# Kernel tuning notes

Hardware: AMD Instinct MI355X
Metric: run time of the kernel (lower is better)

## Reference

```python
import jax, jax.numpy as jnp
import numpy as np

K = 1  # number of items to sample exactly
B, N = 512, 8192


def log1mexp(x):
    # log(1 - exp(x)) for x <= 0, numerically stable (Maechler 2012)
    return jnp.where(x > -jnp.log(2.0), jnp.log(-jnp.expm1(x)), jnp.log1p(-jnp.exp(x)))


def logaddexp_c(x1, x2):
    # custom logaddexp matching the torch module (handles -inf == -inf ties)
    delta = jnp.where(x1 == x2, 0.0, x1 - x2)
    return jnp.maximum(x1, x2) + jax.nn.softplus(-jnp.abs(delta))


def dp_table(logp, logq, kk):
    # a[b, i, c] = log Pr(exactly c-1 successes among first i items); shape [B, n+1, kk+2]
    bsz = logp.shape[0]
    state0 = jnp.full((bsz, kk + 2), -jnp.inf, logp.dtype).at[:, 1].set(0.0)
    ninf_col = jnp.full((bsz, 1), -jnp.inf, logp.dtype)

    def step(state, xs):
        lp, lq = xs  # each [B]
        grown = logaddexp_c(state[:, :-1] + lp[:, None], state[:, 1:] + lq[:, None])
        new = jnp.concatenate([ninf_col, grown], axis=1)
        return new, new

    _, rows = jax.lax.scan(step, state0, (logp.T, logq.T))  # rows: [n, B, kk+2]
    return jnp.concatenate([state0[None], rows], axis=0).transpose(1, 0, 2)


def sample_scan(a, logp, noise):
    # reverse DP sampling pass; a: [B, n+1, C], logp/noise: [B, n]
    bsz, np1, C = a.shape
    n = np1 - 1
    kcol = C - 1  # == K + 1 in table-column coordinates
    ap = a[:, :-1, :][:, ::-1].transpose(1, 0, 2)  # [n, B, C], row i-1 for i=n..1
    ac = a[:, 1:, :][:, ::-1].transpose(1, 0, 2)   # [n, B, C], row i   for i=n..1
    lp_rev = logp[:, ::-1].T                        # [n, B]
    u_rev = noise[:, ::-1].T                        # [n, B]

    def step(j, xs):
        ap_r, ac_r, lp_t, u_t = xs
        p = jnp.take_along_axis(ap_r, (j - 1)[:, None], axis=1)[:, 0]
        z = jnp.take_along_axis(ac_r, j[:, None], axis=1)[:, 0]
        p = jnp.minimum(p + lp_t - z, 0.0)  # conditional log-prob, clamp fp round-off
        q = log1mexp(p)
        X = (u_t < jax.nn.sigmoid(p - q)).astype(logp.dtype)  # Bernoulli(logits=p-q)
        j = jnp.where(X > 0, j - 1, j)
        return j, X

    j0 = jnp.full((bsz,), kcol, jnp.int32)
    _, Xs = jax.lax.scan(step, j0, (ap, ac, lp_rev, u_rev))  # Xs: [n, B]
    return Xs[::-1].T  # [B, n]


def setup_inputs() -> dict:
    key = jax.random.key(0)
    k1, k2 = jax.random.split(key)
    logits = jax.random.normal(k1, (B, N), dtype=jnp.float32)
    noise = jax.random.uniform(k2, (B, N), dtype=jnp.float32)
    return {"logits": logits, "noise": noise}


def reference(logits, noise):
    logp = jnp.minimum(jax.nn.log_sigmoid(logits), -1e-7)  # clamped log_sigmoid
    logq = log1mexp(logp)
    a = dp_table(logp, logq, K)       # [B, N+1, K+2]
    return sample_scan(a, logp, noise)  # [B, N] in {0,1}
```

## Files before the change

### kernel.cpp

```cpp
#include <hip/hip_runtime.h>
#include <math.h>

#define NB 512
#define NI 8192
#define NLOG2 0.69314718055994530942f

__device__ __forceinline__ float log1mexp_f(float x) {
    return (x > -NLOG2) ? logf(-expm1f(x)) : log1pf(-expf(x));
}

__global__ __launch_bounds__(256) void prep_kernel(const float* __restrict__ logits,
                                                   float* __restrict__ Alp,
                                                   float* __restrict__ Blq) {
    int idx = blockIdx.x * blockDim.x + threadIdx.x;
    float4 x4 = ((const float4*)logits)[idx];
    float4 lp4, lq4;
    const float* xs = &x4.x;
    float* lps = &lp4.x;
    float* lqs = &lq4.x;
#pragma unroll
    for (int j = 0; j < 4; ++j) {
        float x = xs[j];
        float lp = -(fmaxf(-x, 0.0f) + log1pf(expf(-fabsf(x))));
        lp = fminf(lp, -1e-7f);
        lps[j] = lp;
        lqs[j] = log1mexp_f(lp);
    }
    ((float4*)Alp)[idx] = lp4;
    ((float4*)Blq)[idx] = lq4;
}

#define CH 32
__device__ __forceinline__ void scan_step(float lp, float lq, float& S0, float& S1,
                                          float& x1o, float& s1o) {
    const float L2E = 1.44269504088896340736f;
    const float LN2 = 0.69314718055994530942f;
    float x1 = S0 + lp;
    float x2 = S1 + lq;
    float d  = x1 - x2;
    float m  = fmaxf(x1, x2);
    float z  = fabsf(d) * -L2E;
    float e  = __builtin_amdgcn_exp2f(z);
    float a  = 1.0f + e;
    float l  = __builtin_amdgcn_logf(a);
    S1 = fmaf(l, LN2, m);
    S0 = S0 + lq;
    x1o = x1;
    s1o = S1;
}

__global__ __launch_bounds__(64, 1) void scan_kernel(float* __restrict__ A,
                                                     float* __restrict__ B) {
    int row = blockIdx.x * blockDim.x + threadIdx.x;
    float* Ar = A + (size_t)row * NI;
    float* Br = B + (size_t)row * NI;

    float S0 = 0.0f;
    float S1 = -INFINITY;

    float lpA[CH], lqA[CH], lpB[CH], lqB[CH];
    float x1A[CH], s1A[CH], x1B[CH], s1B[CH];

#pragma unroll
    for (int j = 0; j < CH / 4; ++j) {
        *(float4*)&lpA[4 * j] = *(const float4*)&Ar[4 * j];
        *(float4*)&lqA[4 * j] = *(const float4*)&Br[4 * j];
    }

    const int NCHUNK = NI / CH;
    for (int c = 0; c < NCHUNK; c += 2) {
        const int base0 = c * CH, base1 = (c + 1) * CH, base2 = (c + 2) * CH;

#pragma unroll
        for (int j = 0; j < CH / 4; ++j) {
            *(float4*)&lpB[4 * j] = *(const float4*)&Ar[base1 + 4 * j];
            *(float4*)&lqB[4 * j] = *(const float4*)&Br[base1 + 4 * j];
        }

#pragma unroll
        for (int j = 0; j < CH; ++j)
            scan_step(lpA[j], lqA[j], S0, S1, x1A[j], s1A[j]);
#pragma unroll
        for (int j = 0; j < CH / 4; ++j) {
            *(float4*)&Ar[base0 + 4 * j] = *(float4*)&x1A[4 * j];
            *(float4*)&Br[base0 + 4 * j] = *(float4*)&s1A[4 * j];
        }

        if (c + 2 < NCHUNK) {
#pragma unroll
            for (int j = 0; j < CH / 4; ++j) {
                *(float4*)&lpA[4 * j] = *(const float4*)&Ar[base2 + 4 * j];
                *(float4*)&lqA[4 * j] = *(const float4*)&Br[base2 + 4 * j];
            }
        }

#pragma unroll
        for (int j = 0; j < CH; ++j)
            scan_step(lpB[j], lqB[j], S0, S1, x1B[j], s1B[j]);
#pragma unroll
        for (int j = 0; j < CH / 4; ++j) {
            *(float4*)&Ar[base1 + 4 * j] = *(float4*)&x1B[4 * j];
            *(float4*)&Br[base1 + 4 * j] = *(float4*)&s1B[4 * j];
        }
    }
}

__global__ __launch_bounds__(256) void decide_kernel(const float* __restrict__ A,
                                                     const float* __restrict__ S,
                                                     const float* __restrict__ noise,
                                                     float* __restrict__ out) {
    int row = blockIdx.x;
    const float4* x1r = (const float4*)(A + (size_t)row * NI);
    const float4* s1r = (const float4*)(S + (size_t)row * NI);
    const float4* ur = (const float4*)(noise + (size_t)row * NI);
    float4* outr = (float4*)(out + (size_t)row * NI);
    int tid = threadIdx.x;

    int best = -1;
#pragma unroll
    for (int k = 0; k < NI / 4 / 256; ++k) {
        int g = tid + k * 256;
        float4 x1 = x1r[g];
        float4 s1 = s1r[g];
        float4 u = ur[g];
#pragma unroll
        for (int j = 0; j < 4; ++j) {
            float p = fminf((&x1.x)[j] - (&s1.x)[j], 0.0f);
            float q = log1mexp_f(p);
            float z = p - q;
            float prob = 1.0f / (1.0f + expf(-z));
            if ((&u.x)[j] < prob) {
                int i = 4 * g + j;
                best = (i > best) ? i : best;
            }
        }
    }

#pragma unroll
    for (int off = 32; off > 0; off >>= 1) {
        int o = __shfl_down(best, off);
        best = (o > best) ? o : best;
    }
    __shared__ int lds[4];
    __shared__ int sel_s;
    int wid = tid >> 6;
    if ((tid & 63) == 0) lds[wid] = best;
    __syncthreads();
    if (tid == 0) {
        int s01 = (lds[0] > lds[1]) ? lds[0] : lds[1];
        int s23 = (lds[2] > lds[3]) ? lds[2] : lds[3];
        sel_s = (s01 > s23) ? s01 : s23;
    }
    __syncthreads();
    int sel = sel_s;

#pragma unroll
    for (int k = 0; k < NI / 4 / 256; ++k) {
        int g = tid + k * 256;
        int i0 = 4 * g;
        float4 v;
        v.x = (i0 == sel) ? 1.0f : 0.0f;
        v.y = (i0 + 1 == sel) ? 1.0f : 0.0f;
        v.z = (i0 + 2 == sel) ? 1.0f : 0.0f;
        v.w = (i0 + 3 == sel) ? 1.0f : 0.0f;
        outr[g] = v;
    }
}

extern "C" void kernel_launch(void* const* d_in, const int* in_sizes, int n_in,
                              void* d_out, int out_size, void* d_ws, size_t ws_size,
                              hipStream_t stream) {
    (void)in_sizes; (void)n_in; (void)out_size; (void)ws_size;
    const float* logits = (const float*)d_in[0];
    const float* noise = (const float*)d_in[1];
    float* out = (float*)d_out;
    float* A = (float*)d_ws;

    int total4 = NB * NI / 4;
    prep_kernel<<<total4 / 256, 256, 0, stream>>>(logits, A, out);
    scan_kernel<<<8, 64, 0, stream>>>(A, out);
    decide_kernel<<<NB, 256, 0, stream>>>(A, out, noise, out);
}
```

Measured before the change: 485.2 us.

## Transpose DP scratch to item-major layout for coalesced scan-kernel access

The prep kernel now transposes log-probabilities through shared memory into an item-major [NI/4][NB] float4 layout. The sequential scan kernel's 64 lanes then read and write adjacent rows, so its memory accesses coalesce instead of being strided by a full row. The decide kernel reads the transposed layout, which is strided per row. The output write is moved into a separate kernel because the decide kernel's reads and the final writes share the out buffer, and the selected index is passed through a global array.

```diff
diff --git a/kernel.cpp b/kernel.cpp
--- a/kernel.cpp
+++ b/kernel.cpp
@@ -3,34 +3,61 @@
 
 #define NB 512
 #define NI 8192
+#define NG (NI / 4)
 #define NLOG2 0.69314718055994530942f
 
 __device__ __forceinline__ float log1mexp_f(float x) {
     return (x > -NLOG2) ? logf(-expm1f(x)) : log1pf(-expf(x));
 }
 
+__device__ int g_sel[NB];
+
+#define TB 64
+#define TK 16
 __global__ __launch_bounds__(256) void prep_kernel(const float* __restrict__ logits,
                                                    float* __restrict__ Alp,
                                                    float* __restrict__ Blq) {
-    int idx = blockIdx.x * blockDim.x + threadIdx.x;
-    float4 x4 = ((const float4*)logits)[idx];
-    float4 lp4, lq4;
-    const float* xs = &x4.x;
-    float* lps = &lp4.x;
-    float* lqs = &lq4.x;
-#pragma unroll
-    for (int j = 0; j < 4; ++j) {
-        float x = xs[j];
-        float lp = -(fmaxf(-x, 0.0f) + log1pf(expf(-fabsf(x))));
-        lp = fminf(lp, -1e-7f);
-        lps[j] = lp;
-        lqs[j] = log1mexp_f(lp);
-    }
-    ((float4*)Alp)[idx] = lp4;
-    ((float4*)Blq)[idx] = lq4;
-}
-
-#define CH 32
+    __shared__ float4 lp_t[TB][TK + 1];
+    __shared__ float4 lq_t[TB][TK + 1];
+    int bx = blockIdx.x;
+    int tb = (bx & 7) * TB;
+    int tkb = (bx >> 3) * TK;
+    int t = threadIdx.x;
+
+    int kl = t & 15;
+    int rl0 = t >> 4;
+#pragma unroll
+    for (int r = 0; r < 4; ++r) {
+        int row_local = r * 16 + rl0;
+        float4 x4 = *(const float4*)&logits[(size_t)(tb + row_local) * NI + (size_t)(tkb + kl) * 4];
+        float4 lp4, lq4;
+        const float* xs = &x4.x;
+        float* lps = &lp4.x;
+        float* lqs = &lq4.x;
+#pragma unroll
+        for (int j = 0; j < 4; ++j) {
+            float x = xs[j];
+            float lp = -(fmaxf(-x, 0.0f) + log1pf(expf(-fabsf(x))));
+            lp = fminf(lp, -1e-7f);
+            lps[j] = lp;
+            lqs[j] = log1mexp_f(lp);
+        }
+        lp_t[row_local][kl] = lp4;
+        lq_t[row_local][kl] = lq4;
+    }
+    __syncthreads();
+
+    int bl = t & 63;
+    int kw0 = t >> 6;
+#pragma unroll
+    for (int w = 0; w < 4; ++w) {
+        int k_local = w * 4 + kw0;
+        size_t dst = (size_t)(tkb + k_local) * NB + (size_t)(tb + bl);
+        ((float4*)Alp)[dst] = lp_t[bl][k_local];
+        ((float4*)Blq)[dst] = lq_t[bl][k_local];
+    }
+}
+
 __device__ __forceinline__ void scan_step(float lp, float lq, float& S0, float& S1,
                                           float& x1o, float& s1o) {
     const float L2E = 1.44269504088896340736f;
@@ -49,79 +76,86 @@
     s1o = S1;
 }
 
+__device__ __forceinline__ void scan_step4(float4 lp, float4 lq, float& S0, float& S1,
+                                           float4& x1v, float4& s1v) {
+    scan_step(lp.x, lq.x, S0, S1, x1v.x, s1v.x);
+    scan_step(lp.y, lq.y, S0, S1, x1v.y, s1v.y);
+    scan_step(lp.z, lq.z, S0, S1, x1v.z, s1v.z);
+    scan_step(lp.w, lq.w, S0, S1, x1v.w, s1v.w);
+}
+
+#define SD 8
 __global__ __launch_bounds__(64, 1) void scan_kernel(float* __restrict__ A,
                                                      float* __restrict__ B) {
-    int row = blockIdx.x * blockDim.x + threadIdx.x;
-    float* Ar = A + (size_t)row * NI;
-    float* Br = B + (size_t)row * NI;
+    int row = blockIdx.x * 64 + threadIdx.x;
+    float4* Ap = (float4*)A;
+    float4* Bp = (float4*)B;
 
     float S0 = 0.0f;
     float S1 = -INFINITY;
 
-    float lpA[CH], lqA[CH], lpB[CH], lqB[CH];
-    float x1A[CH], s1A[CH], x1B[CH], s1B[CH];
-
-#pragma unroll
-    for (int j = 0; j < CH / 4; ++j) {
-        *(float4*)&lpA[4 * j] = *(const float4*)&Ar[4 * j];
-        *(float4*)&lqA[4 * j] = *(const float4*)&Br[4 * j];
-    }
-
-    const int NCHUNK = NI / CH;
+    float4 lpA[SD], lqA[SD], lpB[SD], lqB[SD];
+
+#pragma unroll
+    for (int j = 0; j < SD; ++j) {
+        lpA[j] = Ap[(size_t)j * NB + row];
+        lqA[j] = Bp[(size_t)j * NB + row];
+    }
+
+    const int NCHUNK = NG / SD;
     for (int c = 0; c < NCHUNK; c += 2) {
-        const int base0 = c * CH, base1 = (c + 1) * CH, base2 = (c + 2) * CH;
-
-#pragma unroll
-        for (int j = 0; j < CH / 4; ++j) {
-            *(float4*)&lpB[4 * j] = *(const float4*)&Ar[base1 + 4 * j];
-            *(float4*)&lqB[4 * j] = *(const float4*)&Br[base1 + 4 * j];
-        }
-
-#pragma unroll
-        for (int j = 0; j < CH; ++j)
-            scan_step(lpA[j], lqA[j], S0, S1, x1A[j], s1A[j]);
-#pragma unroll
-        for (int j = 0; j < CH / 4; ++j) {
-            *(float4*)&Ar[base0 + 4 * j] = *(float4*)&x1A[4 * j];
-            *(float4*)&Br[base0 + 4 * j] = *(float4*)&s1A[4 * j];
+        size_t g1 = (size_t)(c + 1) * SD;
+        size_t g2 = (size_t)(c + 2) * SD;
+
+#pragma unroll
+        for (int j = 0; j < SD; ++j) {
+            lpB[j] = Ap[(g1 + j) * NB + row];
+            lqB[j] = Bp[(g1 + j) * NB + row];
+        }
+
+#pragma unroll
+        for (int j = 0; j < SD; ++j) {
+            float4 x1v, s1v;
+            scan_step4(lpA[j], lqA[j], S0, S1, x1v, s1v);
+            size_t g = (size_t)c * SD + j;
+            Ap[g * NB + row] = x1v;
+            Bp[g * NB + row] = s1v;
         }
 
         if (c + 2 < NCHUNK) {
 #pragma unroll
-            for (int j = 0; j < CH / 4; ++j) {
-                *(float4*)&lpA[4 * j] = *(const float4*)&Ar[base2 + 4 * j];
-                *(float4*)&lqA[4 * j] = *(const float4*)&Br[base2 + 4 * j];
+            for (int j = 0; j < SD; ++j) {
+                lpA[j] = Ap[(g2 + j) * NB + row];
+                lqA[j] = Bp[(g2 + j) * NB + row];
             }
         }
 
 #pragma unroll
-        for (int j = 0; j < CH; ++j)
-            scan_step(lpB[j], lqB[j], S0, S1, x1B[j], s1B[j]);
-#pragma unroll
-        for (int j = 0; j < CH / 4; ++j) {
-            *(float4*)&Ar[base1 + 4 * j] = *(float4*)&x1B[4 * j];
-            *(float4*)&Br[base1 + 4 * j] = *(float4*)&s1B[4 * j];
+        for (int j = 0; j < SD; ++j) {
+            float4 x1v, s1v;
+            scan_step4(lpB[j], lqB[j], S0, S1, x1v, s1v);
+            size_t g = g1 + j;
+            Ap[g * NB + row] = x1v;
+            Bp[g * NB + row] = s1v;
         }
     }
 }
 
 __global__ __launch_bounds__(256) void decide_kernel(const float* __restrict__ A,
                                                      const float* __restrict__ S,
-                                                     const float* __restrict__ noise,
-                                                     float* __restrict__ out) {
+                                                     const float* __restrict__ noise) {
     int row = blockIdx.x;
-    const float4* x1r = (const float4*)(A + (size_t)row * NI);
-    const float4* s1r = (const float4*)(S + (size_t)row * NI);
+    const float4* x1p = (const float4*)A;
+    const float4* s1p = (const float4*)S;
     const float4* ur = (const float4*)(noise + (size_t)row * NI);
-    float4* outr = (float4*)(out + (size_t)row * NI);
     int tid = threadIdx.x;
 
     int best = -1;
 #pragma unroll
-    for (int k = 0; k < NI / 4 / 256; ++k) {
+    for (int k = 0; k < NG / 256; ++k) {
         int g = tid + k * 256;
-        float4 x1 = x1r[g];
-        float4 s1 = s1r[g];
+        float4 x1 = x1p[(size_t)g * NB + row];
+        float4 s1 = s1p[(size_t)g * NB + row];
         float4 u = ur[g];
 #pragma unroll
         for (int j = 0; j < 4; ++j) {
@@ -142,20 +176,23 @@
         best = (o > best) ? o : best;
     }
     __shared__ int lds[4];
-    __shared__ int sel_s;
     int wid = tid >> 6;
     if ((tid & 63) == 0) lds[wid] = best;
     __syncthreads();
     if (tid == 0) {
         int s01 = (lds[0] > lds[1]) ? lds[0] : lds[1];
         int s23 = (lds[2] > lds[3]) ? lds[2] : lds[3];
-        sel_s = (s01 > s23) ? s01 : s23;
-    }
-    __syncthreads();
-    int sel = sel_s;
-
-#pragma unroll
-    for (int k = 0; k < NI / 4 / 256; ++k) {
+        g_sel[row] = (s01 > s23) ? s01 : s23;
+    }
+}
+
+__global__ __launch_bounds__(256) void writeout_kernel(float* __restrict__ out) {
+    int row = blockIdx.x;
+    int sel = g_sel[row];
+    float4* outr = (float4*)(out + (size_t)row * NI);
+    int tid = threadIdx.x;
+#pragma unroll
+    for (int k = 0; k < NG / 256; ++k) {
         int g = tid + k * 256;
         int i0 = 4 * g;
         float4 v;
@@ -176,8 +213,8 @@
     float* out = (float*)d_out;
     float* A = (float*)d_ws;
 
-    int total4 = NB * NI / 4;
-    prep_kernel<<<total4 / 256, 256, 0, stream>>>(logits, A, out);
+    prep_kernel<<<8 * (NG / TK), 256, 0, stream>>>(logits, A, out);
     scan_kernel<<<8, 64, 0, stream>>>(A, out);
-    decide_kernel<<<NB, 256, 0, stream>>>(A, out, noise, out);
-}
+    decide_kernel<<<NB, 256, 0, stream>>>(A, out, noise);
+    writeout_kernel<<<NB, 256, 0, stream>>>(out);
+}
```

Result: faster. 408.2 us (-15.9%).
